# Optimization experiments

Measured on AMD Instinct MI355X. Metric: run time of the kernel, lower is better.

Reference implementation:

```python
import jax, jax.numpy as jnp
import numpy as np
from jax import lax

E = 10        # embed_dim
SEQ = 4000    # input_frame (sample_length=40)
G = 800       # group
F = 5         # frames_in_group
B = 16
VOCAB = 8192


def _conv2d(x, w, b):
    # x: [B, C, H, W], w: [O, I, 3, 3], padding=1 -> SAME
    y = lax.conv_general_dilated(x, w, (1, 1), 'SAME',
                                 dimension_numbers=('NCHW', 'OIHW', 'NCHW'))
    return y + b[None, :, None, None]


def _conv1d_k1(x, w, b):
    # Conv1d(seq, seq, kernel=1): x [B, S, L], w [S_out, S_in]
    return jnp.einsum('oi,bil->bol', w, x) + b[None, :, None]


def _linear(x, w, b):
    # torch Linear: w [out, in]
    return x @ w.T + b


def setup_inputs() -> dict:
    key = jax.random.key(0)
    ks = jax.random.split(key, 24)
    s = 0.02
    inp = {
        'X': jax.random.randint(ks[0], (B, SEQ, 15), 0, VOCAB),
        'emb_table': jax.random.normal(ks[1], (VOCAB, E), jnp.float32),
        'w_dwc_lsp': jax.random.normal(ks[2], (G, G, 3, 3), jnp.float32) * s,
        'b_dwc_lsp': jnp.zeros((G,), jnp.float32),
        'w_dwc_other': jax.random.normal(ks[3], (G, G, 3, 3), jnp.float32) * s,
        'b_dwc_other': jnp.zeros((G,), jnp.float32),
        'w_local': jax.random.normal(ks[4], (SEQ, SEQ), jnp.float32) * s,
        'b_local': jnp.zeros((SEQ,), jnp.float32),
        'w_global': jax.random.normal(ks[5], (SEQ, SEQ), jnp.float32) * s,
        'b_global': jnp.zeros((SEQ,), jnp.float32),
        'w_gq': jax.random.normal(ks[6], (4 * E, 4 * E), jnp.float32) * s,
        'b_gq': jnp.zeros((4 * E,), jnp.float32),
        'w_cq': jax.random.normal(ks[7], (4 * E, 4 * E), jnp.float32) * s,
        'b_cq': jnp.zeros((4 * E,), jnp.float32),
        'w_pq': jax.random.normal(ks[8], (4 * E, 3 * E), jnp.float32) * s,
        'b_pq': jnp.zeros((4 * E,), jnp.float32),
        'w_lk': jax.random.normal(ks[9], (4 * E, 4 * E), jnp.float32) * s,
        'b_lk': jnp.zeros((4 * E,), jnp.float32),
        'w_lv': jax.random.normal(ks[10], (4 * E, 4 * E), jnp.float32) * s,
        'b_lv': jnp.zeros((4 * E,), jnp.float32),
        'w_cls': jax.random.normal(ks[11], (1, SEQ * 4 * E * 3), jnp.float32) * 0.001,
        'b_cls': jnp.zeros((1,), jnp.float32),
        'bn_w': jnp.ones((1,), jnp.float32),
        'bn_b': jnp.zeros((1,), jnp.float32),
    }
    return inp


def reference(X, emb_table, w_dwc_lsp, b_dwc_lsp, w_dwc_other, b_dwc_other,
              w_local, b_local, w_global, b_global,
              w_gq, b_gq, w_cq, b_cq, w_pq, b_pq,
              w_lk, b_lk, w_lv, b_lv, w_cls, b_cls, bn_w, bn_b):
    batch, seq, cw = X.shape
    gamma = jnp.float32(0.8)
    pk = jnp.array([0, 0, 0, 0, 1, 3, 1, 2, 3, 2, 3, 1, 2, 3, 3], jnp.float32)
    D = jnp.repeat(gamma ** pk, E)  # [150]

    Xe = emb_table[X].reshape(batch, seq, cw * E) * D  # [B, S, 150]
    ch = Xe.reshape(batch, seq, cw, E)                  # 15 chunks of E

    lsp = ch[:, :, jnp.array([0, 1, 2, 3])].reshape(batch, seq, 4 * E)
    pitch = ch[:, :, jnp.array([4, 5, 10])].reshape(batch, seq, 3 * E)
    code = ch[:, :, jnp.array([6, 7, 11, 12])].reshape(batch, seq, 4 * E)
    gain = ch[:, :, jnp.array([8, 13, 9, 14])].reshape(batch, seq, 4 * E)

    conv_lsp = _conv2d(lsp.reshape(batch, G, F, 4 * E), w_dwc_lsp, b_dwc_lsp).reshape(batch, seq, 4 * E)
    conv_pitch = _conv2d(pitch.reshape(batch, G, F, 3 * E), w_dwc_other, b_dwc_other).reshape(batch, seq, 3 * E)
    conv_code = _conv2d(code.reshape(batch, G, F, 4 * E), w_dwc_other, b_dwc_other).reshape(batch, seq, 4 * E)
    conv_gain = _conv2d(gain.reshape(batch, G, F, 4 * E), w_dwc_other, b_dwc_other).reshape(batch, seq, 4 * E)

    conv_lsp = _conv1d_k1(conv_lsp, w_local, b_local)
    conv_pitch = _conv1d_k1(conv_pitch, w_local, b_local)
    conv_code = _conv1d_k1(conv_code, w_local, b_local)
    conv_gain = _conv1d_k1(conv_gain, w_local, b_local)

    gain_q = _linear(conv_gain, w_gq, b_gq)    # [B, S, 40]
    pitch_q = _linear(conv_pitch, w_pq, b_pq)  # [B, S, 40]
    code_q = _linear(conv_code, w_cq, b_cq)    # [B, S, 40]
    lsp_k = _linear(conv_lsp, w_lk, b_lk)
    lsp_v = _linear(conv_lsp, w_lv, b_lv)

    # Q @ K^T @ V with no softmax: associate as Q @ (K^T V), O(S*d^2)
    kv = jnp.einsum('bsd,bse->bde', lsp_k, lsp_v)  # [B, 40, 40]
    out_gain = jnp.einsum('bsd,bde->bse', gain_q, kv) + lsp
    out_pitch = jnp.einsum('bsd,bde->bse', pitch_q, kv) + lsp
    out_code = jnp.einsum('bsd,bde->bse', code_q, kv) + lsp

    atten_out = jnp.concatenate([out_gain, out_pitch, out_code], -1)  # [B, S, 120]
    gf = _conv1d_k1(atten_out, w_global, b_global).reshape(batch, -1)  # [B, 480000]

    y = gf @ w_cls.T + b_cls  # [B, 1]
    # BatchNorm1d(1) in eval mode: running_mean=0, running_var=1
    eps = jnp.float32(1e-5)
    y = y * (bn_w / jnp.sqrt(1.0 + eps)) + bn_b
    return jax.nn.sigmoid(y)
```

## Files before the change

### kernel.cpp

```cpp
#include <hip/hip_runtime.h>
#include <hip/hip_bf16.h>

typedef _Float16 f16;
typedef __attribute__((ext_vector_type(8))) _Float16 half8;
typedef __attribute__((ext_vector_type(4))) _Float16 half4;
typedef __attribute__((ext_vector_type(4))) float f32x4;

static const int BN = 16, SEQN = 4000;

__device__ __forceinline__ void gload_lds(f16* lds, const f16* g) {
  __builtin_amdgcn_global_load_lds((const __attribute__((address_space(1))) unsigned int*)g,
                                   (__attribute__((address_space(3))) unsigned int*)lds, 16, 0, 0);
}

__device__ __forceinline__ int xcd_swz(int orig, int nwg) {
  int q = nwg >> 3, r = nwg & 7, x = orig & 7, o = orig >> 3;
  return (x < r ? x * (q + 1) : r * (q + 1) + (x - r) * q) + o;
}

__device__ __forceinline__ void body_prepA(char* SM, int bid,
    const float* __restrict__ w_dwc_l, f16* __restrict__ wp_lsp,
    const float* __restrict__ w_local, f16* __restrict__ wlp,
    const float* __restrict__ w_cls, f16* __restrict__ wcT) {
  float* sh = (float*)SM;
  int t = threadIdx.x;
  if (bid < 800) {
    int o = bid;
    for (int p = t; p < 7200; p += 256) sh[p] = w_dwc_l[(long)o * 7200 + p];
    __syncthreads();
    for (int p = t; p < 7296; p += 256) {
      int seg = p / 2432, r = p - seg * 2432;
      f16 v = (f16)0.f;
      if (r < 2400) { int de = r / 800, gi = r % 800; v = (f16)sh[gi * 9 + seg * 3 + de]; }
      wp_lsp[(long)o * 7296 + p] = v;
    }
  } else if (bid < 4800) {
    int s = bid - 800;
    for (int p = t; p < 4000; p += 256) sh[p] = w_local[(long)s * 4000 + p];
    __syncthreads();
    for (int p = t; p < 4096; p += 256) {
      f16 v = (f16)0.f;
      if (p < 4000) { int f = p / 800, g = p % 800; v = (f16)sh[g * 5 + f]; }
      wlp[(long)s * 4096 + p] = v;
    }
  } else {
    int id = bid - 4800;
    int c0 = (id % 4) * 32, r0 = (id / 4) * 32;
    int tx = t & 31, ty = t >> 5;
    float (*tile)[33] = (float(*)[33])SM;
    for (int i = ty; i < 32; i += 8) {
      int r = r0 + i, c = c0 + tx;
      tile[i][tx] = (r < 4000 && c < 120) ? w_cls[(long)r * 120 + c] : 0.f;
    }
    __syncthreads();
    for (int i = ty; i < 32; i += 8) {
      int c = c0 + i, r = r0 + tx;
      if (c < 128 && r < 4000) wcT[(long)c * 4000 + r] = (f16)(tile[tx][i] * 1024.f);
    }
  }
}

__device__ __forceinline__ void body_woT(char* SM, int id,
    const float* __restrict__ in, f16* __restrict__ out) {
  float (*sh)[289] = (float(*)[289])SM;
  int bg = id % 25, bgi = id / 25;
  int g0 = bg * 32, gi0 = bgi * 32;
  int t = threadIdx.x;
  for (int p = t; p < 32 * 288; p += 256) {
    int gl = p / 288, q = p % 288;
    sh[gl][q] = in[(long)(g0 + gl) * 7200 + gi0 * 9 + q];
  }
  __syncthreads();
  for (int p = t; p < 9 * 32 * 32; p += 256) {
    int gl = p & 31, q = p >> 5;
    int gil = q & 31, z = q >> 5;
    out[(long)z * 640000 + (gi0 + gil) * 800 + g0 + gl] = (f16)sh[gl][gil * 9 + z];
  }
}

__device__ __forceinline__ void body_gather(char* SM, int bid,
    const int* __restrict__ X, const float* __restrict__ emb,
    f16* __restrict__ P_lsp, f16* __restrict__ P_pit,
    f16* __restrict__ P_cod, f16* __restrict__ P_gai,
    float* __restrict__ lsp32) {
  int* sx_ = (int*)SM;
  float* slsp = (float*)(SM + 9600);
  const float scale[15] = {1.f,1.f,1.f,1.f,0.8f,0.512f,0.8f,0.64f,0.512f,0.64f,0.512f,0.8f,0.64f,0.512f,0.512f};
  const int br[15] = {0,0,0,0,1,1,2,2,3,3,1,2,2,3,3};
  const int po[15] = {0,1,2,3,0,1,0,1,0,2,2,2,3,1,3};
  int t = threadIdx.x;
  int b = bid / 25, gc = bid % 25;
  int g0 = gc * 32, s0 = g0 * 5;
  const int* xbase = X + ((long)b * SEQN + s0) * 15;
  for (int p = t; p < 2400; p += 256) sx_[p] = xbase[p];
  __syncthreads();
  for (int it = t; it < 2400; it += 256) {
    int gl = it & 31, q = it >> 5, f = q % 5, c = q / 5;
    int idx = sx_[(gl * 5 + f) * 15 + c];
    const float* er = emb + (long)idx * 10;
    int ty = br[c], p = po[c];
    f16* P = (ty == 0) ? P_lsp : (ty == 1) ? P_pit : (ty == 2) ? P_cod : P_gai;
    int Wp = (ty == 1) ? 32 : 42;
    f16* base = P + ((long)((f + 1) * 16 + b) * Wp + (1 + p * 10)) * 800 + g0 + gl;
    float sc = scale[c];
#pragma unroll
    for (int j = 0; j < 10; j++) {
      float v = er[j] * sc;
      base[(long)j * 800] = (f16)v;
      if (ty == 0) slsp[(gl * 5 + f) * 40 + p * 10 + j] = v;
    }
  }
  __syncthreads();
  float* ldst = lsp32 + ((long)b * SEQN + s0) * 40;
  for (int p = t; p < 6400; p += 256) ldst[p] = slsp[p];
}

__device__ __forceinline__ void body_c1(char* SM, int blk,
    const float* __restrict__ wcls, const float* __restrict__ bg,
    float* __restrict__ c1p) {
  float* red = (float*)SM;
  int t = threadIdx.x;
  float s = 0.f;
  for (long i = (long)blk * 256 + t; i < 480000; i += (long)120 * 256)
    s += wcls[i] * bg[i / 120];
  red[t] = s; __syncthreads();
  for (int o = 128; o > 0; o >>= 1) { if (t < o) red[t] += red[t + o]; __syncthreads(); }
  if (t == 0) c1p[blk] = red[0];
}

__device__ __forceinline__ void body_conv(char* SM, int id,
    const f16* __restrict__ P, const f16* __restrict__ wp, float* __restrict__ Cp) {
  f16* Asb = (f16*)SM;
  f16* Bsb = Asb + 8192;
  int lin = xcd_swz(id % 175, 175);
  int z = id / 175;
  int nx = lin % 7, my = lin / 7;
  int m0 = my * 128, n0 = nx * 128;
  Cp += (long)z * 3200 * 800;
  int t = threadIdx.x;
  int gslot = (t & 3) ^ ((t >> 3) & 3);
  const f16 *ap[2], *bp[2];
#pragma unroll
  for (int q = 0; q < 2; q++) {
    int row = q * 64 + (t >> 2);
    int m = m0 + row;
    int f = m / 640, rem = m % 640, b = rem / 40, e = rem % 40;
    ap[q] = P + ((long)((f + z) * 16 + b) * 42 + e) * 800 + gslot * 8;
    bp[q] = wp + (long)(n0 + row) * 7296 + z * 2432 + gslot * 8;
  }
  int lane = t & 63, wv = t >> 6, l15 = lane & 15, kg = lane >> 4;
  int wm = (wv >> 1) * 64, wn = (wv & 1) * 64;
  int so = (kg ^ ((l15 >> 1) & 3)) << 3;
  f32x4 acc[4][4] = {};
  gload_lds(&Asb[t * 8], ap[0]); gload_lds(&Asb[2048 + t * 8], ap[1]);
  gload_lds(&Bsb[t * 8], bp[0]); gload_lds(&Bsb[2048 + t * 8], bp[1]);
  __syncthreads();
  int cur = 0;
  for (int kt = 0; kt < 76; kt++) {
    if (kt + 1 < 76) {
      int o = (kt + 1) * 32, nb = cur ^ 1;
      gload_lds(&Asb[nb * 4096 + t * 8], ap[0] + o); gload_lds(&Asb[nb * 4096 + 2048 + t * 8], ap[1] + o);
      gload_lds(&Bsb[nb * 4096 + t * 8], bp[0] + o); gload_lds(&Bsb[nb * 4096 + 2048 + t * 8], bp[1] + o);
    }
    half8 av[4], bv[4];
#pragma unroll
    for (int i = 0; i < 4; i++) av[i] = *(const half8*)&Asb[cur * 4096 + (wm + i * 16 + l15) * 32 + so];
#pragma unroll
    for (int j = 0; j < 4; j++) bv[j] = *(const half8*)&Bsb[cur * 4096 + (wn + j * 16 + l15) * 32 + so];
#pragma unroll
    for (int i = 0; i < 4; i++)
#pragma unroll
      for (int j = 0; j < 4; j++)
        acc[i][j] = __builtin_amdgcn_mfma_f32_16x16x32_f16(av[i], bv[j], acc[i][j], 0, 0, 0);
    __syncthreads();
    cur ^= 1;
  }
#pragma unroll
  for (int i = 0; i < 4; i++) {
    int mb = m0 + wm + i * 16 + kg * 4;
#pragma unroll
    for (int j = 0; j < 4; j++) {
      int n = n0 + wn + j * 16 + l15;
      if (n >= 800) continue;
      f32x4 d = acc[i][j];
#pragma unroll
      for (int r = 0; r < 4; r++)
        Cp[(long)(mb + r) * 800 + n] = d[r];
    }
  }
}

__device__ __forceinline__ void body_gemm128(char* SM, int x, int ky, int z,
    const f16* __restrict__ A, int lda, const f16* __restrict__ Bm, int ldb,
    float* __restrict__ C, int ldc,
    int gx, int nwg, int nkt, int KTtot, long cslice, long az, long bz, long cz,
    int Mreal, int Nreal, int Aclamp) {
  f16* Asb = (f16*)SM;
  f16* Bsb = Asb + 8192;
  A += (long)z * az;
  Bm += (long)z * bz;
  C += (long)z * cz + (long)ky * cslice;
  int lin = xcd_swz(x, nwg);
  int nx = lin % gx, my = lin / gx;
  int m0 = my * 128, n0 = nx * 128;
  int kt0 = ky * nkt;
  int ktn = nkt; if (kt0 + ktn > KTtot) ktn = KTtot - kt0;
  int t = threadIdx.x;
  int gslot = (t & 3) ^ ((t >> 3) & 3);
  const f16 *ap[2], *bp[2];
#pragma unroll
  for (int q = 0; q < 2; q++) {
    int row = q * 64 + (t >> 2);
    int ra = m0 + row; if (ra >= Aclamp) ra = Aclamp - 1;
    ap[q] = A + (long)ra * lda + (long)kt0 * 32 + gslot * 8;
    bp[q] = Bm + (long)(n0 + row) * ldb + (long)kt0 * 32 + gslot * 8;
  }
  int lane = t & 63, wv = t >> 6, l15 = lane & 15, kg = lane >> 4;
  int wm = (wv >> 1) * 64, wn = (wv & 1) * 64;
  int so = (kg ^ ((l15 >> 1) & 3)) << 3;
  f32x4 acc[4][4] = {};
  gload_lds(&Asb[t * 8], ap[0]); gload_lds(&Asb[2048 + t * 8], ap[1]);
  gload_lds(&Bsb[t * 8], bp[0]); gload_lds(&Bsb[2048 + t * 8], bp[1]);
  __syncthreads();
  int cur = 0;
  for (int kt = 0; kt < ktn; kt++) {
    if (kt + 1 < ktn) {
      int o = (kt + 1) * 32, nb = cur ^ 1;
      gload_lds(&Asb[nb * 4096 + t * 8], ap[0] + o); gload_lds(&Asb[nb * 4096 + 2048 + t * 8], ap[1] + o);
      gload_lds(&Bsb[nb * 4096 + t * 8], bp[0] + o); gload_lds(&Bsb[nb * 4096 + 2048 + t * 8], bp[1] + o);
    }
    half8 av[4], bv[4];
#pragma unroll
    for (int i = 0; i < 4; i++) av[i] = *(const half8*)&Asb[cur * 4096 + (wm + i * 16 + l15) * 32 + so];
#pragma unroll
    for (int j = 0; j < 4; j++) bv[j] = *(const half8*)&Bsb[cur * 4096 + (wn + j * 16 + l15) * 32 + so];
#pragma unroll
    for (int i = 0; i < 4; i++)
#pragma unroll
      for (int j = 0; j < 4; j++)
        acc[i][j] = __builtin_amdgcn_mfma_f32_16x16x32_f16(av[i], bv[j], acc[i][j], 0, 0, 0);
    __syncthreads();
    cur ^= 1;
  }
#pragma unroll
  for (int i = 0; i < 4; i++) {
    int mb = m0 + wm + i * 16 + kg * 4;
#pragma unroll
    for (int j = 0; j < 4; j++) {
      int n = n0 + wn + j * 16 + l15;
      if (n >= Nreal) continue;
      f32x4 d = acc[i][j];
#pragma unroll
      for (int r = 0; r < 4; r++) {
        int m = mb + r;
        if (m >= Mreal) continue;
        C[(long)m * ldc + n] = d[r];
      }
    }
  }
}

__device__ __forceinline__ void body_tn(char* SM, int id,
    const f16* __restrict__ A, int lda, const float* __restrict__ B, int ldb,
    float* __restrict__ C, int ldc, int nkt, int KTtot, long cslice,
    int Mreal, int Nreal) {
  f16* As = (f16*)SM;
  f16* Bs = As + 4096;
  int n0 = (id & 31) * 128;
  int ky = id >> 5;
  int kt0 = ky * nkt;
  int ktn = nkt; if (kt0 + ktn > KTtot) ktn = KTtot - kt0;
  C += (long)ky * cslice;
  int t = threadIdx.x;
  int gslot = (t & 3) ^ ((t >> 3) & 3);
  const f16 *ap0, *ap1;
  {
    int r0 = t >> 2, r1 = 64 + (t >> 2);
    if (r0 >= Mreal) r0 = Mreal - 1;
    if (r1 >= Mreal) r1 = Mreal - 1;
    ap0 = A + (long)r0 * lda + (long)kt0 * 32 + gslot * 8;
    ap1 = A + (long)r1 * lda + (long)kt0 * 32 + gslot * 8;
  }
  int lane = t & 63, wv = t >> 6;
  int wm = (wv >> 1) * 64, wn = (wv & 1) * 64;
  int l15 = lane & 15, kg = lane >> 4;
  int so = (kg ^ ((l15 >> 1) & 3)) << 3;
  f32x4 acc[4][4] = {};
  for (int kt = 0; kt < ktn; kt++) {
    float rb[4][4];
    int nli[4], kqi[4];
#pragma unroll
    for (int i = 0; i < 4; i++) {
      int idd = i * 256 + t;
      nli[i] = idd & 127; kqi[i] = idd >> 7;
      int gn = n0 + nli[i]; if (gn >= Nreal) gn = Nreal - 1;
      long kb = ((long)(kt0 + kt) * 32 + kqi[i] * 4);
#pragma unroll
      for (int j = 0; j < 4; j++) rb[i][j] = B[(kb + j) * ldb + gn];
    }
    __syncthreads();
    gload_lds(&As[t * 8], ap0 + kt * 32);
    gload_lds(&As[2048 + t * 8], ap1 + kt * 32);
#pragma unroll
    for (int i = 0; i < 4; i++) {
      half4 h = {(f16)rb[i][0], (f16)rb[i][1], (f16)rb[i][2], (f16)rb[i][3]};
      *(half4*)&Bs[nli[i] * 36 + kqi[i] * 4] = h;
    }
    __syncthreads();
    half8 av[4], bv[4];
#pragma unroll
    for (int i = 0; i < 4; i++) {
      av[i] = *(const half8*)(&As[(wm + i * 16 + l15) * 32 + so]);
      bv[i] = *(const half8*)(&Bs[(wn + i * 16 + l15) * 36 + kg * 8]);
    }
#pragma unroll
    for (int i = 0; i < 4; i++)
#pragma unroll
      for (int j = 0; j < 4; j++)
        acc[i][j] = __builtin_amdgcn_mfma_f32_16x16x32_f16(av[i], bv[j], acc[i][j], 0, 0, 0);
  }
#pragma unroll
  for (int i = 0; i < 4; i++) {
    int mb = wm + i * 16 + kg * 4;
#pragma unroll
    for (int j = 0; j < 4; j++) {
      int n = n0 + wn + j * 16 + l15;
      if (n >= Nreal) continue;
      f32x4 d = acc[i][j];
#pragma unroll
      for (int r = 0; r < 4; r++) {
        int m = mb + r;
        if (m >= Mreal) continue;
        C[(long)m * ldc + n] = d[r];
      }
    }
  }
}

__device__ __forceinline__ void body_co_red(long gid,
    const float* __restrict__ Cp, const float* __restrict__ bias, f16* __restrict__ co) {
  if (gid >= 640000) return;
  int m = gid / 200, n4 = (gid % 200) * 4;
  long o = (long)m * 800 + n4;
  f32x4 s = *(const f32x4*)&bias[n4];
#pragma unroll
  for (int z = 0; z < 3; z++) s += *(const f32x4*)&Cp[(long)z * 2560000 + o];
  int f = m / 640, r2 = m % 640;
  half4 h = {(f16)s[0], (f16)s[1], (f16)s[2], (f16)s[3]};
  *(half4*)&co[(long)r2 * 4000 + f * 800 + n4] = h;
}

__device__ __forceinline__ void body_vred(int idb, int MODE,
    const float* __restrict__ vp, float* __restrict__ vout, f16* __restrict__ tout) {
  int x = idb & 15, ec = idb >> 4;
  int s = x * 256 + threadIdx.x;
  if (s >= 4000) return;
  int g = s / 5, f = s % 5;
  float sums[40];
#pragma unroll
  for (int eo = 0; eo < 40; eo++) {
    int e = ec * 40 + eo;
    float sum = 0.f;
#pragma unroll
    for (int z = 0; z < 10; z++) sum += vp[(long)z * 480000 + (long)e * 4000 + s];
    sums[eo] = sum;
    if (MODE == 0) tout[(long)e * 4000 + s] = (f16)sum;
    else tout[(long)(f * 120 + e) * 832 + g] = (f16)sum;
  }
#pragma unroll
  for (int q = 0; q < 10; q++)
    *(f32x4*)&vout[(long)s * 120 + ec * 40 + q * 4] = *(f32x4*)&sums[q * 4];
}

__device__ __forceinline__ void body_cl_red(long gid,
    const float* __restrict__ Clp, const float* __restrict__ bl, float* __restrict__ cl) {
  if (gid >= 640000) return;
  int m = gid / 160, n4 = (gid % 160) * 4;
  long o = (long)m * 640 + n4;
  f32x4 s = {0.f, 0.f, 0.f, 0.f};
#pragma unroll
  for (int z = 0; z < 4; z++) s += *(const f32x4*)&Clp[(long)z * 2560000 + o];
  float b = bl[m];
  s += (f32x4){b, b, b, b};
  *(f32x4*)&cl[o] = s;
}

__device__ __forceinline__ void body_resid(char* SM, int chunk, int b,
    const float* __restrict__ lsp32, const float* __restrict__ vmat,
    float* __restrict__ rpart) {
  float* red = (float*)SM;
  int t = threadIdx.x;
  int s0 = chunk * 160;
  float y = 0.f;
  for (int idx = t; idx < 1600; idx += 256) {
    int sr = idx / 10, d4 = idx % 10;
    const float* lp = lsp32 + ((long)b * SEQN + s0 + sr) * 40 + d4 * 4;
    const float* vp = vmat + (long)(s0 + sr) * 120 + d4 * 4;
    f32x4 l = *(const f32x4*)lp;
    f32x4 vs = *(const f32x4*)vp + *(const f32x4*)(vp + 40) + *(const f32x4*)(vp + 80);
    y += l[0] * vs[0] + l[1] * vs[1] + l[2] * vs[2] + l[3] * vs[3];
  }
  red[t] = y; __syncthreads();
  for (int o = 128; o > 0; o >>= 1) { if (t < o) red[t] += red[t + o]; __syncthreads(); }
  if (t == 0) rpart[b * 25 + chunk] = red[0];
}

__device__ __forceinline__ void body_kv(char* SM, int chunk, int b,
    const float* __restrict__ cl, const float* __restrict__ wlk, const float* __restrict__ blk,
    const float* __restrict__ wlv, const float* __restrict__ blv, float* __restrict__ kvp) {
  float* s_wk = (float*)SM;
  float* s_wv = s_wk + 1600;
  float* s_cl = s_wv + 1600;
  float* s_k  = s_cl + 320;
  float* s_v  = s_k + 320;
  int t = threadIdx.x;
  for (int p = t; p < 1600; p += 256) { s_wk[p] = wlk[p]; s_wv[p] = wlv[p]; }
  float acc[7] = {0.f, 0.f, 0.f, 0.f, 0.f, 0.f, 0.f};
  for (int c8 = 0; c8 < 20; c8++) {
    int sb = chunk * 160 + c8 * 8;
    __syncthreads();
    for (int p = t; p < 320; p += 256) {
      int sl = p / 40, e = p % 40;
      s_cl[sl * 40 + e] = cl[(long)(sb + sl) * 640 + b * 40 + e];
    }
    __syncthreads();
    for (int p = t; p < 640; p += 256) {
      int half = p / 320, q = p % 320, sl = q / 40, d = q % 40;
      const float* w = half ? s_wv : s_wk;
      float r = half ? blv[d] : blk[d];
      for (int e = 0; e < 40; e++) r += w[d * 40 + e] * s_cl[sl * 40 + e];
      if (half) s_v[sl * 40 + d] = r; else s_k[sl * 40 + d] = r;
    }
    __syncthreads();
    int ai = 0;
    for (int p = t; p < 1600; p += 256, ai++) {
      int d = p / 40, e = p % 40;
      float a = acc[ai];
      for (int sl = 0; sl < 8; sl++) a += s_k[sl * 40 + d] * s_v[sl * 40 + e];
      acc[ai] = a;
    }
  }
  int ai = 0;
  for (int p = t; p < 1600; p += 256, ai++)
    kvp[((long)(b * 25 + chunk)) * 1600 + p] = acc[ai];
}

__device__ __forceinline__ void body_consts(char* SM, int e,
    const float* __restrict__ Vt, const float* __restrict__ vmat,
    const float* __restrict__ bconv, const float* __restrict__ blocal,
    float* __restrict__ cbblv, float* __restrict__ svv) {
  float* r1 = (float*)SM;
  float* r2 = r1 + 256;
  int t = threadIdx.x;
  float a = 0.f, b = 0.f;
  for (int s = t; s < 4000; s += 256) {
    a += bconv[s / 5] * Vt[(long)s * 120 + e] + blocal[s] * vmat[(long)s * 120 + e];
    b += vmat[(long)s * 120 + e];
  }
  r1[t] = a; r2[t] = b; __syncthreads();
  for (int o = 128; o > 0; o >>= 1) {
    if (t < o) { r1[t] += r1[t + o]; r2[t] += r2[t + o]; }
    __syncthreads();
  }
  if (t == 0) { cbblv[e] = r1[0]; svv[e] = r2[0]; }
}

__device__ __forceinline__ void body_fold(long gid,
    const float* __restrict__ A9, f16* __restrict__ Bp) {
  if (gid >= 7 * 120 * 2496) return;
  int fp = gid / 299520;
  int r = gid % 299520;
  int eg = r / 2496, k2 = r % 2496;
  int zk = k2 / 832, kk = k2 % 832;
  if (kk >= 800) { Bp[gid] = (f16)0.f; return; }
  float s = 0.f;
#pragma unroll
  for (int dh = 0; dh < 3; dh++) {
    int f = fp - dh;
    if (f >= 0 && f < 5)
      s += A9[((long)(dh * 3 + zk) * 640 + f * 120 + eg) * 800 + kk];
  }
  Bp[gid] = (f16)s;
}

__device__ __forceinline__ void body_kvred(long gid,
    const float* __restrict__ kvp, float* __restrict__ kv) {
  if (gid >= 16 * 1600) return;
  int b = gid / 1600, p = gid % 1600;
  float s = 0.f;
  for (int c = 0; c < 25; c++) s += kvp[((long)(b * 25 + c)) * 1600 + p];
  kv[gid] = s;
}

__device__ __forceinline__ void body_U(char* SM, int id,
    const f16* __restrict__ Pg, const f16* __restrict__ Pp, const f16* __restrict__ Pc,
    const f16* __restrict__ Bp, float* __restrict__ Upart) {
  f16* Asb = (f16*)SM;
  f16* Bsb = Asb + 8192;
  int m0 = (id % 28) * 64;
  int y = id / 28, fp = y / 3, zk = y % 3;
  const f16* P; int seg0, jw, Wp, e0;
  if (m0 < 640)       { seg0 = 0;    jw = 40; Wp = 42; e0 = 0;  P = Pg; }
  else if (m0 < 1152) { seg0 = 640;  jw = 30; Wp = 32; e0 = 40; P = Pp; }
  else                { seg0 = 1152; jw = 40; Wp = 42; e0 = 80; P = Pc; }
  P += (long)fp * 16 * Wp * 800;
  int t = threadIdx.x;
  int gslot = (t & 7) ^ ((t >> 3) & 7);
  const f16 *ap[2], *bp[2];
#pragma unroll
  for (int q = 0; q < 2; q++) {
    int row = q * 32 + (t >> 3);
    int l = m0 + row - seg0; if (l >= 16 * jw) l = 0;
    ap[q] = P + ((long)(l / jw) * Wp + (l % jw)) * 800 + (long)zk * 800 + gslot * 8;
    int brow = row; if (e0 + brow > 119) brow = 119 - e0;
    bp[q] = Bp + ((long)fp * 120 + e0 + brow) * 2496 + zk * 832 + gslot * 8;
  }
  int lane = t & 63, wv = t >> 6, l15 = lane & 15, kg = lane >> 4;
  int sx = l15 & 7;
  f32x4 acc[3] = {};
  gload_lds(&Asb[t * 8], ap[0]); gload_lds(&Asb[2048 + t * 8], ap[1]);
  gload_lds(&Bsb[t * 8], bp[0]); gload_lds(&Bsb[2048 + t * 8], bp[1]);
  __syncthreads();
  int cur = 0;
  for (int kt = 0; kt < 13; kt++) {
    if (kt + 1 < 13) {
      int o = (kt + 1) * 64, nb = cur ^ 1;
      gload_lds(&Asb[nb * 4096 + t * 8], ap[0] + o); gload_lds(&Asb[nb * 4096 + 2048 + t * 8], ap[1] + o);
      gload_lds(&Bsb[nb * 4096 + t * 8], bp[0] + o); gload_lds(&Bsb[nb * 4096 + 2048 + t * 8], bp[1] + o);
    }
#pragma unroll
    for (int ks = 0; ks < 2; ks++) {
      int so = ((ks * 4 + kg) ^ sx) << 3;
      half8 av = *(const half8*)&Asb[cur * 4096 + (wv * 16 + l15) * 64 + so];
#pragma unroll
      for (int j = 0; j < 3; j++) {
        half8 bv = *(const half8*)&Bsb[cur * 4096 + (j * 16 + l15) * 64 + so];
        acc[j] = __builtin_amdgcn_mfma_f32_16x16x32_f16(av, bv, acc[j], 0, 0, 0);
      }
    }
    __syncthreads();
    cur ^= 1;
  }
#pragma unroll
  for (int j = 0; j < 3; j++) {
    int n = j * 16 + l15;
    if (n >= 40) continue;
    f32x4 d = acc[j];
#pragma unroll
    for (int r = 0; r < 4; r++) {
      int m = m0 + wv * 16 + kg * 4 + r;
      if (m - seg0 >= 16 * jw) continue;
      Upart[((long)y * 1792 + m) * 40 + n] = d[r];
    }
  }
}

__device__ __forceinline__ void body_ured(long gid,
    const float* __restrict__ Upart, const float* __restrict__ cbblv,
    float* __restrict__ Ufin) {
  if (gid >= 1792 * 40) return;
  int m = gid / 40, e = gid % 40;
  int e0 = m < 640 ? 0 : (m < 1152 ? 40 : 80);
  float s = cbblv[e0 + e];
  for (int y = 0; y < 21; y++) s += Upart[(long)y * 71680 + gid];
  Ufin[gid] = s;
}

__global__ __launch_bounds__(256) void k_phase0(
    const float* w_dwc_l, f16* wp_lsp, const float* w_local, f16* wlp,
    const float* w_cls, f16* wcT, const float* w_dwc_o, f16* woT,
    const int* X, const float* emb, f16* P_lsp, f16* P_pit, f16* P_cod, f16* P_gai,
    float* lsp32, const float* b_global, float* c1p) {
  __shared__ __align__(16) char SM[37120];
  int bid = blockIdx.x;
  if (bid < 5300) body_prepA(SM, bid, w_dwc_l, wp_lsp, w_local, wlp, w_cls, wcT);
  else if (bid < 5925) body_woT(SM, bid - 5300, w_dwc_o, woT);
  else if (bid < 6325) body_gather(SM, bid - 5925, X, emb, P_lsp, P_pit, P_cod, P_gai, lsp32);
  else body_c1(SM, bid - 6325, w_cls, b_global, c1p);
}

__global__ __launch_bounds__(256) void k_phase1(
    const f16* P_lsp, const f16* wp_lsp, float* Cp,
    const f16* wcT, const float* w_global, float* vpart) {
  __shared__ __align__(16) char SM[32768];
  int bid = blockIdx.x;
  if (bid < 525) body_conv(SM, bid, P_lsp, wp_lsp, Cp);
  else body_tn(SM, bid - 525, wcT, 4000, w_global, 4000, vpart, 4000, 13, 125, 480000L, 120, 4000);
}

__global__ __launch_bounds__(256) void k_phase2(
    const float* Cp, const float* b_dwc_l, f16* co,
    const float* vpart, float* vmat, f16* vT) {
  int bid = blockIdx.x;
  if (bid < 2500) body_co_red((long)bid * 256 + threadIdx.x, Cp, b_dwc_l, co);
  else body_vred(bid - 2500, 0, vpart, vmat, vT);
}

__global__ __launch_bounds__(256) void k_phase3(
    const f16* wlp, const f16* co, float* Clp,
    const f16* vT, const float* w_local, float* vpart) {
  __shared__ __align__(16) char SM[32768];
  int bid = blockIdx.x;
  if (bid < 640) body_gemm128(SM, bid % 160, bid / 160, 0, wlp, 4096, co, 4000, Clp, 640,
                              5, 160, 32, 128, 2560000L, 0, 0, 0, 4000, 640, 4000);
  else body_tn(SM, bid - 640, vT, 4000, w_local, 4000, vpart, 4000, 13, 125, 480000L, 120, 4000);
}

__global__ __launch_bounds__(256) void k_phase4(
    const float* Clp, const float* b_local, float* cl,
    const float* vpart, float* Vt, f16* vtT,
    const float* lsp32, const float* vmat, float* rpart) {
  __shared__ __align__(16) char SM[1024];
  int bid = blockIdx.x;
  if (bid < 2500) body_cl_red((long)bid * 256 + threadIdx.x, Clp, b_local, cl);
  else if (bid < 2548) body_vred(bid - 2500, 1, vpart, Vt, vtT);
  else { int id = bid - 2548; body_resid(SM, id % 25, id / 25, lsp32, vmat, rpart); }
}

__global__ __launch_bounds__(256) void k_phase5(
    const float* cl, const float* w_lk, const float* b_lk,
    const float* w_lv, const float* b_lv, float* kvp,
    const f16* vtT, const f16* woT, float* A9,
    const float* Vt, const float* vmat, const float* b_dwc_o, const float* b_local,
    float* cbblv, float* svv) {
  __shared__ __align__(16) char SM[32768];
  int bid = blockIdx.x;
  if (bid < 400) body_kv(SM, bid % 25, bid / 25, cl, w_lk, b_lk, w_lv, b_lv, kvp);
  else if (bid < 715) { int id = bid - 400; body_gemm128(SM, id % 35, 0, id / 35, vtT, 832, woT, 800, A9, 800,
                                                          7, 35, 26, 26, 0L, 0, 640000, 512000, 600, 800, 600); }
  else body_consts(SM, bid - 715, Vt, vmat, b_dwc_o, b_local, cbblv, svv);
}

__global__ __launch_bounds__(256) void k_phase6(
    const float* A9, f16* Bp, const float* kvp, float* kvb) {
  int bid = blockIdx.x;
  if (bid < 8190) body_fold((long)bid * 256 + threadIdx.x, A9, Bp);
  else body_kvred((long)(bid - 8190) * 256 + threadIdx.x, kvp, kvb);
}

__global__ __launch_bounds__(256) void k_phase7(
    const f16* P_gai, const f16* P_pit, const f16* P_cod,
    const f16* Bp, float* Upart) {
  __shared__ __align__(16) char SM[32768];
  body_U(SM, blockIdx.x, P_gai, P_pit, P_cod, Bp, Upart);
}

__global__ __launch_bounds__(256) void k_phase8(
    const float* Upart, const float* cbblv, float* Ufin) {
  body_ured((long)blockIdx.x * 256 + threadIdx.x, Upart, cbblv, Ufin);
}

__global__ __launch_bounds__(256) void k_final(
    const float* __restrict__ Ufin, const float* __restrict__ kvb,
    const float* __restrict__ rpart,
    const float* __restrict__ wgq, const float* __restrict__ wpq, const float* __restrict__ wcq,
    const float* __restrict__ bgq, const float* __restrict__ bpq, const float* __restrict__ bcq,
    const float* __restrict__ svv, const float* __restrict__ c1p,
    const float* __restrict__ bcls, const float* __restrict__ bnw,
    const float* __restrict__ bnb, float* __restrict__ out) {
  __shared__ float s_kv[1600], s_U[4800], s_w[4400], s_bq[120], s_sv[120], s_red[256];
  int b = blockIdx.x, t = threadIdx.x;
  for (int p = t; p < 1600; p += 256) {
    s_kv[p] = kvb[b * 1600 + p];
    s_w[p] = wgq[p];
    s_w[2800 + p] = wcq[p];
  }
  for (int p = t; p < 1200; p += 256) s_w[1600 + p] = wpq[p];
  for (int p = t; p < 4800; p += 256) {
    int tt = p / 1600, r = p % 1600, j = r / 40, e = r % 40;
    float uv = 0.f;
    if (tt == 0) uv = Ufin[(b * 40 + j) * 40 + e];
    else if (tt == 1) { if (j < 30) uv = Ufin[(640 + b * 30 + j) * 40 + e]; }
    else uv = Ufin[(1152 + b * 40 + j) * 40 + e];
    s_U[p] = uv;
  }
  if (t < 40) { s_bq[t] = bgq[t]; s_bq[40 + t] = bpq[t]; s_bq[80 + t] = bcq[t]; }
  for (int p = t; p < 120; p += 256) s_sv[p] = svv[p];
  __syncthreads();
  float y = 0.f;
  for (int p = t; p < 4800; p += 256) {
    int tt = p / 1600, q = p % 1600, d = q / 40, e = q % 40;
    float T = 0.f;
    if (tt == 0) {
      for (int j = 0; j < 40; j++) T += s_w[d * 40 + j] * s_U[j * 40 + e];
    } else if (tt == 1) {
      for (int j = 0; j < 30; j++) T += s_w[1600 + d * 30 + j] * s_U[1600 + j * 40 + e];
    } else {
      for (int j = 0; j < 40; j++) T += s_w[2800 + d * 40 + j] * s_U[3200 + j * 40 + e];
    }
    y += s_kv[d * 40 + e] * (T + s_bq[tt * 40 + d] * s_sv[tt * 40 + e]);
  }
  for (int p = t; p < 25; p += 256) y += rpart[b * 25 + p];
  s_red[t] = y; __syncthreads();
  for (int o = 128; o > 0; o >>= 1) { if (t < o) s_red[t] += s_red[t + o]; __syncthreads(); }
  if (t == 0) {
    float c1 = bcls[0];
    for (int i = 0; i < 120; i++) c1 += c1p[i];
    float yy = s_red[0] * (1.f / 1024.f) + c1;
    yy = yy * (bnw[0] * rsqrtf(1.f + 1e-5f)) + bnb[0];
    out[b] = 1.f / (1.f + expf(-yy));
  }
}

extern "C" void kernel_launch(void* const* d_in, const int* in_sizes, int n_in,
                              void* d_out, int out_size, void* d_ws, size_t ws_size,
                              hipStream_t stream) {
  const int*   X        = (const int*)d_in[0];
  const float* emb      = (const float*)d_in[1];
  const float* w_dwc_l  = (const float*)d_in[2];
  const float* b_dwc_l  = (const float*)d_in[3];
  const float* w_dwc_o  = (const float*)d_in[4];
  const float* b_dwc_o  = (const float*)d_in[5];
  const float* w_local  = (const float*)d_in[6];
  const float* b_local  = (const float*)d_in[7];
  const float* w_global = (const float*)d_in[8];
  const float* b_global = (const float*)d_in[9];
  const float* w_gq = (const float*)d_in[10];
  const float* b_gq = (const float*)d_in[11];
  const float* w_cq = (const float*)d_in[12];
  const float* b_cq = (const float*)d_in[13];
  const float* w_pq = (const float*)d_in[14];
  const float* b_pq = (const float*)d_in[15];
  const float* w_lk = (const float*)d_in[16];
  const float* b_lk = (const float*)d_in[17];
  const float* w_lv = (const float*)d_in[18];
  const float* b_lv = (const float*)d_in[19];
  const float* w_cls = (const float*)d_in[20];
  const float* b_cls = (const float*)d_in[21];
  const float* bn_w = (const float*)d_in[22];
  const float* bn_b = (const float*)d_in[23];
  float* out = (float*)d_out;

  char* ws = (char*)d_ws;
  size_t off = 0;
  auto alloc = [&](size_t bytes) -> void* {
    off = (off + 255) & ~(size_t)255;
    void* p = ws + off; off += bytes; return p;
  };

  const size_t sz_p40 = (size_t)7 * 16 * 42 * 800 * 2;
  const size_t sz_p30 = (size_t)7 * 16 * 32 * 800 * 2;
  f16* P_lsp = (f16*)alloc(sz_p40 + 256);
  f16* P_pit = (f16*)alloc(sz_p30 + 256);
  f16* P_cod = (f16*)alloc(sz_p40 + 256);
  f16* P_gai = (f16*)alloc(sz_p40 + 256);
  float* lsp32 = (float*)alloc((size_t)16 * 4000 * 40 * 4);
  f16* wp_lsp = (f16*)alloc((size_t)896 * 7296 * 2);
  f16* wlp    = (f16*)alloc((size_t)4000 * 4096 * 2 + 256);
  f16* wcT    = (f16*)alloc((size_t)128 * 4000 * 2);
  f16* vT     = (f16*)alloc((size_t)128 * 4000 * 2);
  f16* co     = (f16*)alloc((size_t)640 * 4000 * 2 + 256);
  float* cl   = (float*)alloc((size_t)4000 * 640 * 4);
  float* vmat  = (float*)alloc((size_t)480000 * 4);
  float* Vt    = (float*)alloc((size_t)480000 * 4);
  f16* vtT   = (f16*)alloc((size_t)640 * 832 * 2 + 256);
  f16* Bp    = (f16*)alloc((size_t)7 * 120 * 2496 * 2);
  float* Upart = (float*)alloc((size_t)21 * 1792 * 40 * 4);
  float* Ufin  = (float*)alloc((size_t)1792 * 40 * 4);
  float* cbblv = (float*)alloc(120 * 4);
  float* svv   = (float*)alloc(120 * 4);
  float* kvp  = (float*)alloc((size_t)400 * 1600 * 4);
  float* kvb  = (float*)alloc((size_t)16 * 1600 * 4);
  float* c1p  = (float*)alloc(120 * 4);
  float* rpart = (float*)alloc(400 * 4);
  f16* woT = (f16*)alloc(((size_t)9 * 640000 + 76800) * 2);
  float* vpart = (float*)alloc((size_t)10 * 480000 * 4);
  char* arena = (char*)alloc((size_t)41 * 1024 * 1024);
  float* Cp  = (float*)arena;
  float* Clp = (float*)arena;
  float* A9  = (float*)arena;
  (void)ws_size; (void)in_sizes; (void)n_in; (void)out_size;

  hipMemsetAsync(P_lsp, 0, sz_p40, stream);
  hipMemsetAsync(P_pit, 0, sz_p30, stream);
  hipMemsetAsync(P_cod, 0, sz_p40, stream);
  hipMemsetAsync(P_gai, 0, sz_p40, stream);
  hipMemsetAsync(vtT, 0, (size_t)640 * 832 * 2, stream);

  k_phase0<<<6445, 256, 0, stream>>>(w_dwc_l, wp_lsp, w_local, wlp, w_cls, wcT,
                                     w_dwc_o, woT, X, emb, P_lsp, P_pit, P_cod, P_gai,
                                     lsp32, b_global, c1p);
  k_phase1<<<845, 256, 0, stream>>>(P_lsp, wp_lsp, Cp, wcT, w_global, vpart);
  k_phase2<<<2548, 256, 0, stream>>>(Cp, b_dwc_l, co, vpart, vmat, vT);
  k_phase3<<<960, 256, 0, stream>>>(wlp, co, Clp, vT, w_local, vpart);
  k_phase4<<<2948, 256, 0, stream>>>(Clp, b_local, cl, vpart, Vt, vtT, lsp32, vmat, rpart);
  k_phase5<<<835, 256, 0, stream>>>(cl, w_lk, b_lk, w_lv, b_lv, kvp,
                                    vtT, woT, A9, Vt, vmat, b_dwc_o, b_local, cbblv, svv);
  k_phase6<<<8290, 256, 0, stream>>>(A9, Bp, kvp, kvb);
  k_phase7<<<588, 256, 0, stream>>>(P_gai, P_pit, P_cod, Bp, Upart);
  k_phase8<<<280, 256, 0, stream>>>(Upart, cbblv, Ufin);
  k_final<<<16, 256, 0, stream>>>(Ufin, kvb, rpart,
                                  w_gq, w_pq, w_cq, b_gq, b_pq, b_cq,
                                  svv, c1p, b_cls, bn_w, bn_b, out);
}
```

Baseline: 468.5 us.

## Vectorize weight repacking and redistribute prep work across later phases

Weight repacking (conv, local, woT), the X gather load, the lsp store and the fold step now use 16-byte vector loads and half8 stores instead of scalar accesses, which cuts the number of memory instructions. The w_local repack moves into phase1, the woT repack into phase2 and the residual computation into phase3, so that independent work runs alongside the GEMMs. This shrinks the phase0 grid and leaves other launches less underfilled. The larger shared-memory footprint in phase2 could lower occupancy for the reduction blocks in that launch.

```diff
diff --git a/kernel.cpp b/kernel.cpp
--- a/kernel.cpp
+++ b/kernel.cpp
@@ -18,63 +18,80 @@
   return (x < r ? x * (q + 1) : r * (q + 1) + (x - r) * q) + o;
 }
 
-__device__ __forceinline__ void body_prepA(char* SM, int bid,
-    const float* __restrict__ w_dwc_l, f16* __restrict__ wp_lsp,
-    const float* __restrict__ w_local, f16* __restrict__ wlp,
+__device__ __forceinline__ void body_wconv(char* SM, int o,
+    const float* __restrict__ w_dwc_l, f16* __restrict__ wp_lsp) {
+  float* sh = (float*)SM;
+  int t = threadIdx.x;
+  for (int p4 = t; p4 < 1800; p4 += 256)
+    *(f32x4*)&sh[p4 * 4] = *(const f32x4*)&w_dwc_l[(long)o * 7200 + p4 * 4];
+  __syncthreads();
+  for (int c = t; c < 912; c += 256) {
+    int p = c * 8;
+    int seg = p / 2432, r = p - seg * 2432;
+    half8 h = {};
+    if (r < 2400) {
+      int de = r / 800, gib = r - de * 800;
+#pragma unroll
+      for (int j = 0; j < 8; j++) h[j] = (f16)sh[(gib + j) * 9 + seg * 3 + de];
+    }
+    *(half8*)&wp_lsp[(long)o * 7296 + p] = h;
+  }
+}
+
+__device__ __forceinline__ void body_wlocal(char* SM, int s,
+    const float* __restrict__ w_local, f16* __restrict__ wlp) {
+  float* sh = (float*)SM;
+  int t = threadIdx.x;
+  for (int p4 = t; p4 < 1000; p4 += 256)
+    *(f32x4*)&sh[p4 * 4] = *(const f32x4*)&w_local[(long)s * 4000 + p4 * 4];
+  __syncthreads();
+  for (int c = t; c < 512; c += 256) {
+    int p = c * 8;
+    half8 h = {};
+    if (p < 4000) {
+      int f = p / 800, g = p - f * 800;
+#pragma unroll
+      for (int j = 0; j < 8; j++) h[j] = (f16)sh[(g + j) * 5 + f];
+    }
+    *(half8*)&wlp[(long)s * 4096 + p] = h;
+  }
+}
+
+__device__ __forceinline__ void body_wcT(char* SM, int id,
     const float* __restrict__ w_cls, f16* __restrict__ wcT) {
-  float* sh = (float*)SM;
-  int t = threadIdx.x;
-  if (bid < 800) {
-    int o = bid;
-    for (int p = t; p < 7200; p += 256) sh[p] = w_dwc_l[(long)o * 7200 + p];
-    __syncthreads();
-    for (int p = t; p < 7296; p += 256) {
-      int seg = p / 2432, r = p - seg * 2432;
-      f16 v = (f16)0.f;
-      if (r < 2400) { int de = r / 800, gi = r % 800; v = (f16)sh[gi * 9 + seg * 3 + de]; }
-      wp_lsp[(long)o * 7296 + p] = v;
-    }
-  } else if (bid < 4800) {
-    int s = bid - 800;
-    for (int p = t; p < 4000; p += 256) sh[p] = w_local[(long)s * 4000 + p];
-    __syncthreads();
-    for (int p = t; p < 4096; p += 256) {
-      f16 v = (f16)0.f;
-      if (p < 4000) { int f = p / 800, g = p % 800; v = (f16)sh[g * 5 + f]; }
-      wlp[(long)s * 4096 + p] = v;
-    }
-  } else {
-    int id = bid - 4800;
-    int c0 = (id % 4) * 32, r0 = (id / 4) * 32;
-    int tx = t & 31, ty = t >> 5;
-    float (*tile)[33] = (float(*)[33])SM;
-    for (int i = ty; i < 32; i += 8) {
-      int r = r0 + i, c = c0 + tx;
-      tile[i][tx] = (r < 4000 && c < 120) ? w_cls[(long)r * 120 + c] : 0.f;
-    }
-    __syncthreads();
-    for (int i = ty; i < 32; i += 8) {
-      int c = c0 + i, r = r0 + tx;
-      if (c < 128 && r < 4000) wcT[(long)c * 4000 + r] = (f16)(tile[tx][i] * 1024.f);
-    }
+  float (*tile)[33] = (float(*)[33])SM;
+  int t = threadIdx.x;
+  int c0 = (id % 4) * 32, r0 = (id / 4) * 32;
+  int tx = t & 31, ty = t >> 5;
+  for (int i = ty; i < 32; i += 8) {
+    int r = r0 + i, c = c0 + tx;
+    tile[i][tx] = (r < 4000 && c < 120) ? w_cls[(long)r * 120 + c] : 0.f;
+  }
+  __syncthreads();
+  for (int i = ty; i < 32; i += 8) {
+    int c = c0 + i, r = r0 + tx;
+    if (c < 128 && r < 4000) wcT[(long)c * 4000 + r] = (f16)(tile[tx][i] * 1024.f);
   }
 }
 
 __device__ __forceinline__ void body_woT(char* SM, int id,
     const float* __restrict__ in, f16* __restrict__ out) {
-  float (*sh)[289] = (float(*)[289])SM;
+  float (*sh)[292] = (float(*)[292])SM;
   int bg = id % 25, bgi = id / 25;
   int g0 = bg * 32, gi0 = bgi * 32;
   int t = threadIdx.x;
-  for (int p = t; p < 32 * 288; p += 256) {
-    int gl = p / 288, q = p % 288;
-    sh[gl][q] = in[(long)(g0 + gl) * 7200 + gi0 * 9 + q];
-  }
-  __syncthreads();
-  for (int p = t; p < 9 * 32 * 32; p += 256) {
-    int gl = p & 31, q = p >> 5;
+  for (int p = t; p < 2304; p += 256) {
+    int gl = p / 72, q4 = p % 72;
+    *(f32x4*)&sh[gl][q4 * 4] = *(const f32x4*)&in[(long)(g0 + gl) * 7200 + gi0 * 9 + q4 * 4];
+  }
+  __syncthreads();
+  for (int c = t; c < 1152; c += 256) {
+    int gl8 = c & 3, q = c >> 2;
     int gil = q & 31, z = q >> 5;
-    out[(long)z * 640000 + (gi0 + gil) * 800 + g0 + gl] = (f16)sh[gl][gil * 9 + z];
+    half8 h;
+#pragma unroll
+    for (int j = 0; j < 8; j++) h[j] = (f16)sh[gl8 * 8 + j][gil * 9 + z];
+    *(half8*)&out[(long)z * 640000 + (gi0 + gil) * 800 + g0 + gl8 * 8] = h;
   }
 }
 
@@ -92,7 +109,8 @@
   int b = bid / 25, gc = bid % 25;
   int g0 = gc * 32, s0 = g0 * 5;
   const int* xbase = X + ((long)b * SEQN + s0) * 15;
-  for (int p = t; p < 2400; p += 256) sx_[p] = xbase[p];
+  for (int p = t; p < 600; p += 256)
+    *(f32x4*)&sx_[p * 4] = *(const f32x4*)&xbase[p * 4];
   __syncthreads();
   for (int it = t; it < 2400; it += 256) {
     int gl = it & 31, q = it >> 5, f = q % 5, c = q / 5;
@@ -112,7 +130,8 @@
   }
   __syncthreads();
   float* ldst = lsp32 + ((long)b * SEQN + s0) * 40;
-  for (int p = t; p < 6400; p += 256) ldst[p] = slsp[p];
+  for (int p4 = t; p4 < 1600; p4 += 256)
+    *(f32x4*)&ldst[p4 * 4] = *(const f32x4*)&slsp[p4 * 4];
 }
 
 __device__ __forceinline__ void body_c1(char* SM, int blk,
@@ -465,22 +484,29 @@
   if (t == 0) { cbblv[e] = r1[0]; svv[e] = r2[0]; }
 }
 
-__device__ __forceinline__ void body_fold(long gid,
+__device__ __forceinline__ void body_fold(long c8,
     const float* __restrict__ A9, f16* __restrict__ Bp) {
-  if (gid >= 7 * 120 * 2496) return;
-  int fp = gid / 299520;
-  int r = gid % 299520;
+  long p = c8 * 8;
+  if (p >= 7 * 120 * 2496) return;
+  int fp = p / 299520;
+  int r = p % 299520;
   int eg = r / 2496, k2 = r % 2496;
   int zk = k2 / 832, kk = k2 % 832;
-  if (kk >= 800) { Bp[gid] = (f16)0.f; return; }
-  float s = 0.f;
-#pragma unroll
-  for (int dh = 0; dh < 3; dh++) {
-    int f = fp - dh;
-    if (f >= 0 && f < 5)
-      s += A9[((long)(dh * 3 + zk) * 640 + f * 120 + eg) * 800 + kk];
-  }
-  Bp[gid] = (f16)s;
+  half8 h = {};
+  if (kk < 800) {
+#pragma unroll
+    for (int j = 0; j < 8; j++) {
+      float s = 0.f;
+#pragma unroll
+      for (int dh = 0; dh < 3; dh++) {
+        int f = fp - dh;
+        if (f >= 0 && f < 5)
+          s += A9[((long)(dh * 3 + zk) * 640 + f * 120 + eg) * 800 + kk + j];
+      }
+      h[j] = (f16)s;
+    }
+  }
+  *(half8*)&Bp[p] = h;
 }
 
 __device__ __forceinline__ void body_kvred(long gid,
@@ -567,54 +593,57 @@
 }
 
 __global__ __launch_bounds__(256) void k_phase0(
-    const float* w_dwc_l, f16* wp_lsp, const float* w_local, f16* wlp,
-    const float* w_cls, f16* wcT, const float* w_dwc_o, f16* woT,
+    const float* w_dwc_l, f16* wp_lsp, const float* w_cls, f16* wcT,
     const int* X, const float* emb, f16* P_lsp, f16* P_pit, f16* P_cod, f16* P_gai,
     float* lsp32, const float* b_global, float* c1p) {
-  __shared__ __align__(16) char SM[37120];
+  __shared__ __align__(16) char SM[35200];
   int bid = blockIdx.x;
-  if (bid < 5300) body_prepA(SM, bid, w_dwc_l, wp_lsp, w_local, wlp, w_cls, wcT);
-  else if (bid < 5925) body_woT(SM, bid - 5300, w_dwc_o, woT);
-  else if (bid < 6325) body_gather(SM, bid - 5925, X, emb, P_lsp, P_pit, P_cod, P_gai, lsp32);
-  else body_c1(SM, bid - 6325, w_cls, b_global, c1p);
+  if (bid < 800) body_wconv(SM, bid, w_dwc_l, wp_lsp);
+  else if (bid < 1300) body_wcT(SM, bid - 800, w_cls, wcT);
+  else if (bid < 1700) body_gather(SM, bid - 1300, X, emb, P_lsp, P_pit, P_cod, P_gai, lsp32);
+  else body_c1(SM, bid - 1700, w_cls, b_global, c1p);
 }
 
 __global__ __launch_bounds__(256) void k_phase1(
     const f16* P_lsp, const f16* wp_lsp, float* Cp,
-    const f16* wcT, const float* w_global, float* vpart) {
+    const f16* wcT, const float* w_global, float* vpart,
+    const float* w_local, f16* wlp) {
   __shared__ __align__(16) char SM[32768];
   int bid = blockIdx.x;
   if (bid < 525) body_conv(SM, bid, P_lsp, wp_lsp, Cp);
-  else body_tn(SM, bid - 525, wcT, 4000, w_global, 4000, vpart, 4000, 13, 125, 480000L, 120, 4000);
+  else if (bid < 845) body_tn(SM, bid - 525, wcT, 4000, w_global, 4000, vpart, 4000, 13, 125, 480000L, 120, 4000);
+  else body_wlocal(SM, bid - 845, w_local, wlp);
 }
 
 __global__ __launch_bounds__(256) void k_phase2(
     const float* Cp, const float* b_dwc_l, f16* co,
-    const float* vpart, float* vmat, f16* vT) {
+    const float* vpart, float* vmat, f16* vT,
+    const float* w_dwc_o, f16* woT) {
+  __shared__ __align__(16) char SM[37376];
   int bid = blockIdx.x;
   if (bid < 2500) body_co_red((long)bid * 256 + threadIdx.x, Cp, b_dwc_l, co);
-  else body_vred(bid - 2500, 0, vpart, vmat, vT);
+  else if (bid < 2548) body_vred(bid - 2500, 0, vpart, vmat, vT);
+  else body_woT(SM, bid - 2548, w_dwc_o, woT);
 }
 
 __global__ __launch_bounds__(256) void k_phase3(
     const f16* wlp, const f16* co, float* Clp,
-    const f16* vT, const float* w_local, float* vpart) {
+    const f16* vT, const float* w_local, float* vpart,
+    const float* lsp32, const float* vmat, float* rpart) {
   __shared__ __align__(16) char SM[32768];
   int bid = blockIdx.x;
   if (bid < 640) body_gemm128(SM, bid % 160, bid / 160, 0, wlp, 4096, co, 4000, Clp, 640,
                               5, 160, 32, 128, 2560000L, 0, 0, 0, 4000, 640, 4000);
-  else body_tn(SM, bid - 640, vT, 4000, w_local, 4000, vpart, 4000, 13, 125, 480000L, 120, 4000);
+  else if (bid < 960) body_tn(SM, bid - 640, vT, 4000, w_local, 4000, vpart, 4000, 13, 125, 480000L, 120, 4000);
+  else { int id = bid - 960; body_resid(SM, id % 25, id / 25, lsp32, vmat, rpart); }
 }
 
 __global__ __launch_bounds__(256) void k_phase4(
     const float* Clp, const float* b_local, float* cl,
-    const float* vpart, float* Vt, f16* vtT,
-    const float* lsp32, const float* vmat, float* rpart) {
-  __shared__ __align__(16) char SM[1024];
+    const float* vpart, float* Vt, f16* vtT) {
   int bid = blockIdx.x;
   if (bid < 2500) body_cl_red((long)bid * 256 + threadIdx.x, Clp, b_local, cl);
-  else if (bid < 2548) body_vred(bid - 2500, 1, vpart, Vt, vtT);
-  else { int id = bid - 2548; body_resid(SM, id % 25, id / 25, lsp32, vmat, rpart); }
+  else body_vred(bid - 2500, 1, vpart, Vt, vtT);
 }
 
 __global__ __launch_bounds__(256) void k_phase5(
@@ -634,8 +663,8 @@
 __global__ __launch_bounds__(256) void k_phase6(
     const float* A9, f16* Bp, const float* kvp, float* kvb) {
   int bid = blockIdx.x;
-  if (bid < 8190) body_fold((long)bid * 256 + threadIdx.x, A9, Bp);
-  else body_kvred((long)(bid - 8190) * 256 + threadIdx.x, kvp, kvb);
+  if (bid < 1024) body_fold((long)bid * 256 + threadIdx.x, A9, Bp);
+  else body_kvred((long)(bid - 1024) * 256 + threadIdx.x, kvp, kvb);
 }
 
 __global__ __launch_bounds__(256) void k_phase7(
@@ -777,16 +806,17 @@
   hipMemsetAsync(P_gai, 0, sz_p40, stream);
   hipMemsetAsync(vtT, 0, (size_t)640 * 832 * 2, stream);
 
-  k_phase0<<<6445, 256, 0, stream>>>(w_dwc_l, wp_lsp, w_local, wlp, w_cls, wcT,
-                                     w_dwc_o, woT, X, emb, P_lsp, P_pit, P_cod, P_gai,
+  k_phase0<<<1820, 256, 0, stream>>>(w_dwc_l, wp_lsp, w_cls, wcT,
+                                     X, emb, P_lsp, P_pit, P_cod, P_gai,
                                      lsp32, b_global, c1p);
-  k_phase1<<<845, 256, 0, stream>>>(P_lsp, wp_lsp, Cp, wcT, w_global, vpart);
-  k_phase2<<<2548, 256, 0, stream>>>(Cp, b_dwc_l, co, vpart, vmat, vT);
-  k_phase3<<<960, 256, 0, stream>>>(wlp, co, Clp, vT, w_local, vpart);
-  k_phase4<<<2948, 256, 0, stream>>>(Clp, b_local, cl, vpart, Vt, vtT, lsp32, vmat, rpart);
+  k_phase1<<<4845, 256, 0, stream>>>(P_lsp, wp_lsp, Cp, wcT, w_global, vpart,
+                                     w_local, wlp);
+  k_phase2<<<3173, 256, 0, stream>>>(Cp, b_dwc_l, co, vpart, vmat, vT, w_dwc_o, woT);
+  k_phase3<<<1360, 256, 0, stream>>>(wlp, co, Clp, vT, w_local, vpart, lsp32, vmat, rpart);
+  k_phase4<<<2548, 256, 0, stream>>>(Clp, b_local, cl, vpart, Vt, vtT);
   k_phase5<<<835, 256, 0, stream>>>(cl, w_lk, b_lk, w_lv, b_lv, kvp,
                                     vtT, woT, A9, Vt, vmat, b_dwc_o, b_local, cbblv, svv);
-  k_phase6<<<8290, 256, 0, stream>>>(A9, Bp, kvp, kvb);
+  k_phase6<<<1124, 256, 0, stream>>>(A9, Bp, kvp, kvb);
   k_phase7<<<588, 256, 0, stream>>>(P_gai, P_pit, P_cod, Bp, Upart);
   k_phase8<<<280, 256, 0, stream>>>(Upart, cbblv, Ufin);
   k_final<<<16, 256, 0, stream>>>(Ufin, kvb, rpart,
```

Result: faster. 456.0 us (-2.7%).
